# Kernel optimization log

Measured on AMD Instinct MI355X. Metric: run time of the kernel, lower is better.

Reference implementation:

```python
import jax, jax.numpy as jnp
import numpy as np
import math

M_FEAT = 8  # module-level m = 4 * 2


def theta(u, R):
    # Performer FAVOR random feature map: [cos(uR), sin(uR)] / sqrt(m)
    p = u @ R  # [b, t, m]
    return jnp.concatenate([jnp.cos(p), jnp.sin(p)], axis=-1) / math.sqrt(M_FEAT)


def setup_inputs() -> dict:
    key = jax.random.key(0)
    ks = jax.random.split(key, 8)
    n_embd, n_head = 1024, 16
    d_head = n_embd // n_head  # 64
    b, t = 4, 8192
    x = jax.random.normal(ks[0], (b, t, n_embd), dtype=jnp.float32)
    # random feature projection buffer w: [d_head, m]
    w = jax.random.normal(ks[1], (d_head, M_FEAT), dtype=jnp.float32)
    # nn.Linear(n_embd, d_head) weights (stored as [in, out] for x @ W) + biases
    s = 1.0 / math.sqrt(n_embd)
    Wq = jax.random.uniform(ks[2], (n_embd, d_head), minval=-s, maxval=s, dtype=jnp.float32)
    bq = jax.random.uniform(ks[3], (d_head,), minval=-s, maxval=s, dtype=jnp.float32)
    Wk = jax.random.uniform(ks[4], (n_embd, d_head), minval=-s, maxval=s, dtype=jnp.float32)
    bk = jax.random.uniform(ks[5], (d_head,), minval=-s, maxval=s, dtype=jnp.float32)
    Wv = jax.random.uniform(ks[6], (n_embd, d_head), minval=-s, maxval=s, dtype=jnp.float32)
    bv = jax.random.uniform(ks[7], (d_head,), minval=-s, maxval=s, dtype=jnp.float32)
    return {"x": x, "w": w, "Wq": Wq, "bq": bq, "Wk": Wk, "bk": bk, "Wv": Wv, "bv": bv}


def reference(x, w, Wq, bq, Wk, bk, Wv, bv):
    # Projections to per-head dim
    q = x @ Wq + bq  # [b, t, d_head]
    k = x @ Wk + bk
    v = x @ Wv + bv
    # FAVOR+ random feature maps (features concatenated on last dim)
    qP = theta(q, w)  # [b, t, 2m]
    Kp = theta(k, w)  # [b, t, 2m]
    # Linear attention: S = Kp^T @ V, then y = qP @ S  (O(t) instead of O(t^2))
    S = jnp.einsum('btm,btd->bmd', Kp, v)   # [b, 2m, d_head]
    y = jnp.einsum('btm,bmd->btd', qP, S)   # [b, t, d_head]
    return y
```

## Files before the change

kernel.cpp:

```cpp
#include <hip/hip_runtime.h>
#include <cstdint>

#define E_DIM 1024
#define NROWS 32768
#define LDT 1028
#define INV_SQRT8 0.35355339059327373f

typedef __bf16 bf16x8 __attribute__((ext_vector_type(8)));
typedef float f32x4 __attribute__((ext_vector_type(4)));
typedef const __attribute__((address_space(1))) void* gas_t;
typedef __attribute__((address_space(3))) void* las_t;

__global__ __launch_bounds__(256) void favor_setup(
    const float* __restrict__ w,
    const float* __restrict__ Wq,
    const float* __restrict__ bq,
    const float* __restrict__ Wk,
    const float* __restrict__ bk,
    const float* __restrict__ Wv,
    float* __restrict__ bqw,
    float* __restrict__ bkw,
    __bf16* __restrict__ WpHS,
    __bf16* __restrict__ WpLS,
    __bf16* __restrict__ WvS)
{
    const int g = blockIdx.x * 256 + threadIdx.x;
    {
        const int k = g >> 4;
        const int c = g & 15;
        const float* Wsrc = (c < 8) ? Wq : Wk;
        const int cc = c & 7;
        float s = 0.f;
        #pragma unroll 8
        for (int d = 0; d < 64; ++d)
            s += Wsrc[k * 64 + d] * w[d * 8 + cc];
        const __bf16 h = (__bf16)s;
        const int step = k >> 5, quad = (k >> 3) & 3, j = k & 7;
        const int lane = quad * 16 + c;
        const int idx = (step * 64 + lane) * 8 + j;
        WpHS[idx] = h;
        WpLS[idx] = (__bf16)(s - (float)h);
    }
    #pragma unroll
    for (int t = 0; t < 4; ++t) {
        const int idx = g * 4 + t;
        const int n = idx >> 10;
        const int k = idx & 1023;
        const int ct = n >> 4, l15 = n & 15;
        const int step = k >> 5, quad = (k >> 3) & 3, j = k & 7;
        const int lane = quad * 16 + l15;
        WvS[(((ct * 32 + step) * 64) + lane) * 8 + j] = (__bf16)Wv[k * 64 + n];
    }
    if (g < 16) {
        const int col = g & 7;
        const float* bb = (g < 8) ? bq : bk;
        float s1 = 0.f;
        #pragma unroll 8
        for (int d = 0; d < 64; ++d)
            s1 += bb[d] * w[d * 8 + col];
        if (g < 8) bqw[col] = s1; else bkw[col] = s1;
    }
}

__global__ __launch_bounds__(256, 2) void favor_main(
    const float* __restrict__ x,
    const __bf16* __restrict__ WvS,
    const __bf16* __restrict__ WpHS,
    const __bf16* __restrict__ WpLS,
    const float* __restrict__ bqw,
    const float* __restrict__ bkw,
    const float* __restrict__ bv,
    float* __restrict__ pq_out,
    float* __restrict__ Sbkt)
{
    __shared__ __align__(16) float smem[16 * LDT];
    float* bufW = smem;
    float* vb   = smem + 4096;
    float* kp   = smem + 5248;
    float* sred = smem + 5632;

    const int tid  = threadIdx.x;
    const int wg   = blockIdx.x;
    const int lane = tid & 63;
    const int wv   = __builtin_amdgcn_readfirstlane(tid >> 6);
    const int l15  = lane & 15;
    const int quad = lane >> 4;

    {
        const int sr = wv * 4;
        const float* xs = x + ((long)wg * 16 + sr) * E_DIM + lane * 4;
        #pragma unroll
        for (int r = 0; r < 4; ++r)
            #pragma unroll
            for (int c = 0; c < 4; ++c)
                __builtin_amdgcn_global_load_lds(
                    (gas_t)(xs + r * E_DIM + c * 256),
                    (las_t)(smem + (sr + r) * LDT + c * 256), 16, 0, 0);
    }

    f32x4 zero = {0.f, 0.f, 0.f, 0.f};
    f32x4 accv[4];
    #pragma unroll
    for (int ct = 0; ct < 4; ++ct) accv[ct] = zero;
    f32x4 accp = zero;

    __syncthreads();

    const int cb = wv * 256;
    #pragma unroll
    for (int ks = 0; ks < 8; ++ks) {
        const float* ap = smem + l15 * LDT + cb + ks * 32 + quad * 8;
        const float4 a0 = *(const float4*)ap;
        const float4 a1 = *(const float4*)(ap + 4);
        bf16x8 ah, al;
        {
            const float f[8] = {a0.x, a0.y, a0.z, a0.w, a1.x, a1.y, a1.z, a1.w};
            #pragma unroll
            for (int i = 0; i < 8; ++i) {
                const __bf16 h = (__bf16)f[i];
                ah[i] = h; al[i] = (__bf16)(f[i] - (float)h);
            }
        }
        const int gs = wv * 8 + ks;
        const __bf16* bp = WvS + (long)gs * 512 + lane * 8;
        #pragma unroll
        for (int ct = 0; ct < 4; ++ct) {
            const bf16x8 b = *(const bf16x8*)(bp + ct * 16384);
            accv[ct] = __builtin_amdgcn_mfma_f32_16x16x32_bf16(ah, b, accv[ct], 0, 0, 0);
        }
        {
            const bf16x8 bh = *(const bf16x8*)(WpHS + (long)gs * 512 + lane * 8);
            const bf16x8 bl = *(const bf16x8*)(WpLS + (long)gs * 512 + lane * 8);
            accp = __builtin_amdgcn_mfma_f32_16x16x32_bf16(ah, bh, accp, 0, 0, 0);
            accp = __builtin_amdgcn_mfma_f32_16x16x32_bf16(al, bh, accp, 0, 0, 0);
            accp = __builtin_amdgcn_mfma_f32_16x16x32_bf16(ah, bl, accp, 0, 0, 0);
        }
    }
    __syncthreads();

    if (wv != 0) {
        float* dst = bufW + ((wv - 1) * 64 + lane) * 20;
        #pragma unroll
        for (int ct = 0; ct < 4; ++ct)
            *(f32x4*)(dst + ct * 4) = accv[ct];
        *(f32x4*)(dst + 16) = accp;
    }
    __syncthreads();
    if (wv == 0) {
        #pragma unroll
        for (int j = 0; j < 3; ++j) {
            const float* src = bufW + (j * 64 + lane) * 20;
            #pragma unroll
            for (int ct = 0; ct < 4; ++ct)
                accv[ct] += *(const f32x4*)(src + ct * 4);
            accp += *(const f32x4*)(src + 16);
        }
        if (l15 < 8) {
            const float bq_ = bqw[l15];
            #pragma unroll
            for (int r = 0; r < 4; ++r) {
                const long gr = (long)wg * 16 + quad * 4 + r;
                pq_out[gr * 8 + l15] = accp[r] + bq_;
            }
        } else {
            const float bk_ = bkw[l15 - 8];
            #pragma unroll
            for (int r = 0; r < 4; ++r) {
                const int lr = quad * 4 + r;
                const float pk_ = accp[r] + bk_;
                kp[lr * 16 + (l15 - 8)] = __cosf(pk_) * INV_SQRT8;
                kp[lr * 16 + l15]       = __sinf(pk_) * INV_SQRT8;
            }
        }
        #pragma unroll
        for (int ct = 0; ct < 4; ++ct) {
            const float bv_ = bv[ct * 16 + l15];
            #pragma unroll
            for (int r = 0; r < 4; ++r)
                vb[(quad * 4 + r) * 68 + ct * 16 + l15] = accv[ct][r] + bv_;
        }
    }
    __syncthreads();

    {
        const int d4 = l15;
        const int mg = quad;
        const int rq = wv;
        float sa[16];
        #pragma unroll
        for (int i = 0; i < 16; ++i) sa[i] = 0.f;
        #pragma unroll
        for (int rr = 0; rr < 4; ++rr) {
            const int r = rq * 4 + rr;
            const float4 vv  = *(const float4*)(vb + r * 68 + d4 * 4);
            const float4 kk4 = *(const float4*)(kp + r * 16 + mg * 4);
            const float km[4] = {kk4.x, kk4.y, kk4.z, kk4.w};
            const float vm[4] = {vv.x, vv.y, vv.z, vv.w};
            #pragma unroll
            for (int mi = 0; mi < 4; ++mi)
                #pragma unroll
                for (int di = 0; di < 4; ++di)
                    sa[mi * 4 + di] += km[mi] * vm[di];
        }
        if (rq > 0) {
            float* dst = sred + ((rq - 1) * 64 + lane) * 20;
            #pragma unroll
            for (int i = 0; i < 4; ++i)
                *(float4*)(dst + i * 4) = make_float4(sa[i*4], sa[i*4+1], sa[i*4+2], sa[i*4+3]);
        }
        __syncthreads();
        if (rq == 0) {
            #pragma unroll
            for (int j = 0; j < 3; ++j) {
                const float* src = sred + (j * 64 + lane) * 20;
                #pragma unroll
                for (int i = 0; i < 16; ++i) sa[i] += src[i];
            }
            float* Sb = Sbkt + ((long)(wg & 127) * 4 + (wg >> 9)) * 1024;
            #pragma unroll
            for (int mi = 0; mi < 4; ++mi)
                #pragma unroll
                for (int di = 0; di < 4; ++di)
                    atomicAdd(&Sb[(mg * 4 + mi) * 64 + d4 * 4 + di], sa[mi * 4 + di]);
        }
    }
}

__global__ __launch_bounds__(256) void favor_reduce(
    const float* __restrict__ Sbkt,
    float* __restrict__ S)
{
    const int g = blockIdx.x * 256 + threadIdx.x;
    const int b = g >> 10;
    const int col = g & 1023;
    float s = 0.f;
    #pragma unroll 8
    for (int j = 0; j < 128; ++j)
        s += Sbkt[((long)j * 4 + b) * 1024 + col];
    S[b * 1024 + col] = s;
}

__global__ __launch_bounds__(256) void favor_out(
    const float* __restrict__ pq,
    const float* __restrict__ S,
    float* __restrict__ y)
{
    __shared__ __align__(16) float Ly[64 * 68];

    const int tid = threadIdx.x;
    const int blk = blockIdx.x;
    const int lane = tid & 63;
    const int w = __builtin_amdgcn_readfirstlane(tid >> 6);
    const long row = (long)blk * 64 + lane;
    const int b = blk >> 7;

    const float4 p0 = *(const float4*)(pq + row * 8);
    const float4 p1 = *(const float4*)(pq + row * 8 + 4);
    float qp[16];
    qp[0] = __cosf(p0.x) * INV_SQRT8;  qp[1] = __cosf(p0.y) * INV_SQRT8;
    qp[2] = __cosf(p0.z) * INV_SQRT8;  qp[3] = __cosf(p0.w) * INV_SQRT8;
    qp[4] = __cosf(p1.x) * INV_SQRT8;  qp[5] = __cosf(p1.y) * INV_SQRT8;
    qp[6] = __cosf(p1.z) * INV_SQRT8;  qp[7] = __cosf(p1.w) * INV_SQRT8;
    qp[8] = __sinf(p0.x) * INV_SQRT8;  qp[9] = __sinf(p0.y) * INV_SQRT8;
    qp[10]= __sinf(p0.z) * INV_SQRT8;  qp[11]= __sinf(p0.w) * INV_SQRT8;
    qp[12]= __sinf(p1.x) * INV_SQRT8;  qp[13]= __sinf(p1.y) * INV_SQRT8;
    qp[14]= __sinf(p1.z) * INV_SQRT8;  qp[15]= __sinf(p1.w) * INV_SQRT8;

    const float* Sb = S + b * 1024 + w * 16;
    float a[16];
    #pragma unroll
    for (int i = 0; i < 16; ++i) a[i] = 0.f;
    #pragma unroll
    for (int m = 0; m < 16; ++m) {
        const float4 s0 = *(const float4*)(Sb + m * 64);
        const float4 s1 = *(const float4*)(Sb + m * 64 + 4);
        const float4 s2 = *(const float4*)(Sb + m * 64 + 8);
        const float4 s3 = *(const float4*)(Sb + m * 64 + 12);
        const float qm = qp[m];
        a[0] += qm * s0.x;  a[1] += qm * s0.y;  a[2] += qm * s0.z;  a[3] += qm * s0.w;
        a[4] += qm * s1.x;  a[5] += qm * s1.y;  a[6] += qm * s1.z;  a[7] += qm * s1.w;
        a[8] += qm * s2.x;  a[9] += qm * s2.y;  a[10]+= qm * s2.z;  a[11]+= qm * s2.w;
        a[12]+= qm * s3.x;  a[13]+= qm * s3.y;  a[14]+= qm * s3.z;  a[15]+= qm * s3.w;
    }
    {
        float* lw = Ly + lane * 68 + w * 16;
        *(float4*)(lw)      = make_float4(a[0],  a[1],  a[2],  a[3]);
        *(float4*)(lw + 4)  = make_float4(a[4],  a[5],  a[6],  a[7]);
        *(float4*)(lw + 8)  = make_float4(a[8],  a[9],  a[10], a[11]);
        *(float4*)(lw + 12) = make_float4(a[12], a[13], a[14], a[15]);
    }
    __syncthreads();
    {
        const float* ls = Ly + (w * 16 + (lane >> 4)) * 68 + (lane & 15) * 4;
        float* yb = y + (long)blk * 4096 + w * 1024 + lane * 4;
        #pragma unroll
        for (int i = 0; i < 4; ++i) {
            const float4 v = *(const float4*)(ls + i * 4 * 68);
            *(float4*)(yb + i * 256) = v;
        }
    }
}

extern "C" void kernel_launch(void* const* d_in, const int* in_sizes, int n_in,
                              void* d_out, int out_size, void* d_ws, size_t ws_size,
                              hipStream_t stream) {
    const float* x  = (const float*)d_in[0];
    const float* w  = (const float*)d_in[1];
    const float* Wq = (const float*)d_in[2];
    const float* bq = (const float*)d_in[3];
    const float* Wk = (const float*)d_in[4];
    const float* bk = (const float*)d_in[5];
    const float* Wv = (const float*)d_in[6];
    const float* bv = (const float*)d_in[7];
    float* y = (float*)d_out;

    char* ws = (char*)d_ws;
    float*  S    = (float*)(ws);
    float*  bqw  = (float*)(ws + 16384);
    float*  bkw  = (float*)(ws + 16448);
    __bf16* WpHS = (__bf16*)(ws + 32768);
    __bf16* WpLS = (__bf16*)(ws + 65536);
    __bf16* WvS  = (__bf16*)(ws + 98304);
    float*  Sbkt = (float*)(ws + 229376);
    float*  pq   = (float*)(ws + 2326528);

    hipMemsetAsync(Sbkt, 0, 128 * 4 * 1024 * sizeof(float), stream);
    favor_setup<<<64, 256, 0, stream>>>(w, Wq, bq, Wk, bk, Wv, bqw, bkw, WpHS, WpLS, WvS);
    favor_main<<<2048, 256, 0, stream>>>(x, WvS, WpHS, WpLS, bqw, bkw, bv, pq, Sbkt);
    favor_reduce<<<16, 256, 0, stream>>>(Sbkt, S);
    favor_out<<<512, 256, 0, stream>>>(pq, S, y);
}
```

Measured before the change: 260.6 us.

## Double-buffer x tiles in LDS, raise occupancy, replace S atomics with per-block partials

The main kernel now streams the 16x1024 x tile in four 256-column chunks through two smaller LDS buffers, so the next chunk's global-to-LDS load overlaps the current chunk's MFMA work. Shrinking LDS lets launch bounds ask for 4 workgroups per CU instead of 2. Per-block S partials are written with plain vector stores into a 2048-slot buffer instead of atomics into 128 buckets, which removes the memset. The reduce kernel is widened to 64 blocks that sum 512 partials per batch. The cost is more barriers per block, extra partial-buffer traffic and a longer reduction.

```diff
diff --git a/kernel.cpp b/kernel.cpp
--- a/kernel.cpp
+++ b/kernel.cpp
@@ -3,7 +3,7 @@
 
 #define E_DIM 1024
 #define NROWS 32768
-#define LDT 1028
+#define LDT 260
 #define INV_SQRT8 0.35355339059327373f
 
 typedef __bf16 bf16x8 __attribute__((ext_vector_type(8)));
@@ -62,7 +62,7 @@
     }
 }
 
-__global__ __launch_bounds__(256, 2) void favor_main(
+__global__ __launch_bounds__(256, 4) void favor_main(
     const float* __restrict__ x,
     const __bf16* __restrict__ WvS,
     const __bf16* __restrict__ WpHS,
@@ -73,11 +73,13 @@
     float* __restrict__ pq_out,
     float* __restrict__ Sbkt)
 {
-    __shared__ __align__(16) float smem[16 * LDT];
+    __shared__ __align__(16) float smem[2 * 16 * LDT];
+    float* buf0 = smem;
+    float* buf1 = smem + 16 * LDT;
     float* bufW = smem;
-    float* vb   = smem + 4096;
-    float* kp   = smem + 5248;
-    float* sred = smem + 5632;
+    float* vb   = smem + 3840;
+    float* kp   = smem + 4928;
+    float* sred = smem + 5248;
 
     const int tid  = threadIdx.x;
     const int wg   = blockIdx.x;
@@ -86,17 +88,15 @@
     const int l15  = lane & 15;
     const int quad = lane >> 4;
 
-    {
-        const int sr = wv * 4;
-        const float* xs = x + ((long)wg * 16 + sr) * E_DIM + lane * 4;
-        #pragma unroll
-        for (int r = 0; r < 4; ++r)
-            #pragma unroll
-            for (int c = 0; c < 4; ++c)
-                __builtin_amdgcn_global_load_lds(
-                    (gas_t)(xs + r * E_DIM + c * 256),
-                    (las_t)(smem + (sr + r) * LDT + c * 256), 16, 0, 0);
-    }
+    const float* xs = x + ((long)wg * 16 + wv * 4) * E_DIM + lane * 4;
+    const int ldsrow = wv * 4;
+
+#define PF(buf, s)                                                             \
+    _Pragma("unroll")                                                          \
+    for (int r = 0; r < 4; ++r)                                                \
+        __builtin_amdgcn_global_load_lds(                                      \
+            (gas_t)(xs + r * E_DIM + (s) * 256),                               \
+            (las_t)((buf) + (ldsrow + r) * LDT), 16, 0, 0);
 
     f32x4 zero = {0.f, 0.f, 0.f, 0.f};
     f32x4 accv[4];
@@ -104,39 +104,48 @@
     for (int ct = 0; ct < 4; ++ct) accv[ct] = zero;
     f32x4 accp = zero;
 
-    __syncthreads();
-
-    const int cb = wv * 256;
-    #pragma unroll
-    for (int ks = 0; ks < 8; ++ks) {
-        const float* ap = smem + l15 * LDT + cb + ks * 32 + quad * 8;
-        const float4 a0 = *(const float4*)ap;
-        const float4 a1 = *(const float4*)(ap + 4);
-        bf16x8 ah, al;
-        {
-            const float f[8] = {a0.x, a0.y, a0.z, a0.w, a1.x, a1.y, a1.z, a1.w};
-            #pragma unroll
-            for (int i = 0; i < 8; ++i) {
-                const __bf16 h = (__bf16)f[i];
-                ah[i] = h; al[i] = (__bf16)(f[i] - (float)h);
-            }
-        }
-        const int gs = wv * 8 + ks;
-        const __bf16* bp = WvS + (long)gs * 512 + lane * 8;
-        #pragma unroll
-        for (int ct = 0; ct < 4; ++ct) {
-            const bf16x8 b = *(const bf16x8*)(bp + ct * 16384);
-            accv[ct] = __builtin_amdgcn_mfma_f32_16x16x32_bf16(ah, b, accv[ct], 0, 0, 0);
-        }
-        {
-            const bf16x8 bh = *(const bf16x8*)(WpHS + (long)gs * 512 + lane * 8);
-            const bf16x8 bl = *(const bf16x8*)(WpLS + (long)gs * 512 + lane * 8);
-            accp = __builtin_amdgcn_mfma_f32_16x16x32_bf16(ah, bh, accp, 0, 0, 0);
-            accp = __builtin_amdgcn_mfma_f32_16x16x32_bf16(al, bh, accp, 0, 0, 0);
-            accp = __builtin_amdgcn_mfma_f32_16x16x32_bf16(ah, bl, accp, 0, 0, 0);
-        }
-    }
-    __syncthreads();
+    PF(buf0, 0)
+    __syncthreads();
+
+    #pragma unroll
+    for (int s = 0; s < 4; ++s) {
+        float* wb = (s & 1) ? buf1 : buf0;
+        if (s < 3) {
+            float* nb = (s & 1) ? buf0 : buf1;
+            PF(nb, s + 1)
+        }
+        #pragma unroll
+        for (int ks = 0; ks < 2; ++ks) {
+            const float* ap = wb + l15 * LDT + wv * 64 + ks * 32 + quad * 8;
+            const float4 a0 = *(const float4*)ap;
+            const float4 a1 = *(const float4*)(ap + 4);
+            bf16x8 ah, al;
+            {
+                const float f[8] = {a0.x, a0.y, a0.z, a0.w, a1.x, a1.y, a1.z, a1.w};
+                #pragma unroll
+                for (int i = 0; i < 8; ++i) {
+                    const __bf16 h = (__bf16)f[i];
+                    ah[i] = h; al[i] = (__bf16)(f[i] - (float)h);
+                }
+            }
+            const int gs = s * 8 + wv * 2 + ks;
+            const __bf16* bp = WvS + (long)gs * 512 + lane * 8;
+            #pragma unroll
+            for (int ct = 0; ct < 4; ++ct) {
+                const bf16x8 b = *(const bf16x8*)(bp + ct * 16384);
+                accv[ct] = __builtin_amdgcn_mfma_f32_16x16x32_bf16(ah, b, accv[ct], 0, 0, 0);
+            }
+            {
+                const bf16x8 bh = *(const bf16x8*)(WpHS + (long)gs * 512 + lane * 8);
+                const bf16x8 bl = *(const bf16x8*)(WpLS + (long)gs * 512 + lane * 8);
+                accp = __builtin_amdgcn_mfma_f32_16x16x32_bf16(ah, bh, accp, 0, 0, 0);
+                accp = __builtin_amdgcn_mfma_f32_16x16x32_bf16(al, bh, accp, 0, 0, 0);
+                accp = __builtin_amdgcn_mfma_f32_16x16x32_bf16(ah, bl, accp, 0, 0, 0);
+            }
+        }
+        __syncthreads();
+    }
+#undef PF
 
     if (wv != 0) {
         float* dst = bufW + ((wv - 1) * 64 + lane) * 20;
@@ -183,6 +192,7 @@
     __syncthreads();
 
     {
+        float* sredo = smem;
         const int d4 = l15;
         const int mg = quad;
         const int rq = wv;
@@ -203,7 +213,7 @@
                     sa[mi * 4 + di] += km[mi] * vm[di];
         }
         if (rq > 0) {
-            float* dst = sred + ((rq - 1) * 64 + lane) * 20;
+            float* dst = sredo + ((rq - 1) * 64 + lane) * 20;
             #pragma unroll
             for (int i = 0; i < 4; ++i)
                 *(float4*)(dst + i * 4) = make_float4(sa[i*4], sa[i*4+1], sa[i*4+2], sa[i*4+3]);
@@ -212,16 +222,15 @@
         if (rq == 0) {
             #pragma unroll
             for (int j = 0; j < 3; ++j) {
-                const float* src = sred + (j * 64 + lane) * 20;
+                const float* src = sredo + (j * 64 + lane) * 20;
                 #pragma unroll
                 for (int i = 0; i < 16; ++i) sa[i] += src[i];
             }
-            float* Sb = Sbkt + ((long)(wg & 127) * 4 + (wg >> 9)) * 1024;
+            float* Sb = Sbkt + (long)wg * 1024;
             #pragma unroll
             for (int mi = 0; mi < 4; ++mi)
-                #pragma unroll
-                for (int di = 0; di < 4; ++di)
-                    atomicAdd(&Sb[(mg * 4 + mi) * 64 + d4 * 4 + di], sa[mi * 4 + di]);
+                *(float4*)(Sb + (mg * 4 + mi) * 64 + d4 * 4) =
+                    make_float4(sa[mi*4], sa[mi*4+1], sa[mi*4+2], sa[mi*4+3]);
         }
     }
 }
@@ -230,14 +239,21 @@
     const float* __restrict__ Sbkt,
     float* __restrict__ S)
 {
-    const int g = blockIdx.x * 256 + threadIdx.x;
-    const int b = g >> 10;
-    const int col = g & 1023;
+    __shared__ float red[3][64];
+    const int b  = blockIdx.x >> 4;
+    const int cc = blockIdx.x & 15;
+    const int c  = threadIdx.x & 63;
+    const int jq = threadIdx.x >> 6;
+    const int col = cc * 64 + c;
+    const float* base = Sbkt + ((long)b * 512 + jq * 128) * 1024 + col;
     float s = 0.f;
-    #pragma unroll 8
+    #pragma unroll 16
     for (int j = 0; j < 128; ++j)
-        s += Sbkt[((long)j * 4 + b) * 1024 + col];
-    S[b * 1024 + col] = s;
+        s += base[(long)j * 1024];
+    if (jq > 0) red[jq - 1][c] = s;
+    __syncthreads();
+    if (jq == 0)
+        S[b * 1024 + col] = s + red[0][c] + red[1][c] + red[2][c];
 }
 
 __global__ __launch_bounds__(256) void favor_out(
@@ -322,11 +338,10 @@
     __bf16* WpLS = (__bf16*)(ws + 65536);
     __bf16* WvS  = (__bf16*)(ws + 98304);
     float*  Sbkt = (float*)(ws + 229376);
-    float*  pq   = (float*)(ws + 2326528);
-
-    hipMemsetAsync(Sbkt, 0, 128 * 4 * 1024 * sizeof(float), stream);
+    float*  pq   = (float*)(ws + 8617984);
+
     favor_setup<<<64, 256, 0, stream>>>(w, Wq, bq, Wk, bk, Wv, bqw, bkw, WpHS, WpLS, WvS);
     favor_main<<<2048, 256, 0, stream>>>(x, WvS, WpHS, WpLS, bqw, bkw, bv, pq, Sbkt);
-    favor_reduce<<<16, 256, 0, stream>>>(Sbkt, S);
+    favor_reduce<<<64, 256, 0, stream>>>(Sbkt, S);
     favor_out<<<512, 256, 0, stream>>>(pq, S, y);
 }
```

After: 227.1 us. 12.8% less time.
